# Performance work log

Hardware: AMD Instinct MI355X
Metric: run time of the kernel (lower is better)

## Reference

```python
import jax, jax.numpy as jnp
import numpy as np

N = 50000      # nodes
E = 1600000    # edges (avg degree 32)
IN = 128       # input feature dim
H = 4          # heads
C = 16         # out channels per head
NEG_SLOPE = 0.2


def setup_inputs() -> dict:
    key = jax.random.key(0)
    k = jax.random.split(key, 6)
    x = jax.random.normal(k[0], (N, IN), jnp.float32)
    edge_index = jax.random.randint(k[1], (2, E), 0, N, dtype=jnp.int32).astype(jnp.int64)
    W = jax.random.normal(k[2], (H * C, IN), jnp.float32) * (1.0 / np.sqrt(IN))
    att_src = jax.random.normal(k[3], (H, C), jnp.float32) * 0.1
    att_dst = jax.random.normal(k[4], (H, C), jnp.float32) * 0.1
    bias = jax.random.normal(k[5], (H * C,), jnp.float32) * 0.01
    return {"x": x, "edge_index": edge_index, "W": W,
            "att_src": att_src, "att_dst": att_dst, "bias": bias}


def reference(x, edge_index, W, att_src, att_dst, bias):
    # shared linear projection (PyG GATConv lin, no bias): [N, H, C]
    xp = (x @ W.T).reshape(-1, H, C)
    # per-node attention logits: [N, H]
    a_src = jnp.einsum('nhc,hc->nh', xp, att_src)
    a_dst = jnp.einsum('nhc,hc->nh', xp, att_dst)
    src, dst = edge_index[0], edge_index[1]  # messages flow src(j) -> dst(i)
    # per-edge scores: [E, H]
    e = jax.nn.leaky_relu(a_src[src] + a_dst[dst], negative_slope=NEG_SLOPE)
    # segment softmax over destination neighborhoods
    m = jax.ops.segment_max(e, dst, num_segments=N)           # [N, H]
    m = jnp.where(jnp.isfinite(m), m, 0.0)                     # empty segments
    ex = jnp.exp(e - m[dst])
    s = jax.ops.segment_sum(ex, dst, num_segments=N)           # [N, H]
    alpha = ex / (s[dst] + 1e-16)                              # [E, H]
    # weighted messages, scatter-add to destinations
    msg = (alpha[:, :, None] * xp[src]).reshape(E, H * C)      # [E, H*C]
    out = jax.ops.segment_sum(msg, dst, num_segments=N)        # [N, H*C]
    return out + bias
```

## Files before the change

kernel.cpp:

```cpp
#include <hip/hip_runtime.h>
#include <hip/hip_bf16.h>
#include <math.h>

#define N_NODES 50000
#define N_EDGES 1600000
#define IN_DIM  128
#define HC      64
#define NH      4
#define SLOTS   72
#define BSHIFT  6
#define BNODES  64
#define NB      782
#define BCAP    2432
#define EPB     2736
#define GEMM_BLOCKS 391
#define FAT_GRID 587
#define FAT_LDS 33792

__global__ __launch_bounds__(512) void gemm_bucket_kernel(
    const float* __restrict__ x, const float* __restrict__ W,
    const float* __restrict__ att_src, const float* __restrict__ att_dst,
    const int* __restrict__ ei,
    __hip_bfloat16* __restrict__ xp, float* __restrict__ a_src,
    float* __restrict__ a_dst,
    int* __restrict__ gcursor, unsigned int* __restrict__ barr) {
    extern __shared__ char smraw[];
    int tid = (int)threadIdx.x;
    int bx  = (int)blockIdx.x;

    {
        int* lcount = (int*)smraw;
        int* lbase  = lcount + NB;
        for (int j = tid; j < NB; j += 512) lcount[j] = 0;
        __syncthreads();
        int s[6], d[6], bk[6], lpos[6]; bool val[6];
#pragma unroll
        for (int u = 0; u < 6; ++u) {
            int off = u * 512 + tid;
            int e   = bx * EPB + off;
            val[u]  = (off < EPB) && (e < N_EDGES);
            int ee  = val[u] ? e : 0;
            s[u] = ei[ee];
            d[u] = ei[N_EDGES + ee];
            bk[u] = d[u] >> BSHIFT;
            if (val[u]) lpos[u] = atomicAdd(&lcount[bk[u]], 1);
        }
        __syncthreads();
        for (int j = tid; j < NB; j += 512) {
            int c = lcount[j];
            lbase[j] = (c > 0) ? atomicAdd(&gcursor[j], c) : 0;
        }
        __syncthreads();
#pragma unroll
        for (int u = 0; u < 6; ++u) {
            if (val[u]) {
                int pos = lbase[bk[u]] + lpos[u];
                if (pos < BCAP)
                    barr[(size_t)bk[u] * BCAP + pos] =
                        (unsigned)s[u] | ((unsigned)(d[u] & (BNODES - 1)) << 20);
            }
        }
    }

    if (bx < GEMM_BLOCKS) {
        __syncthreads();
        int gb = bx;
        float* Wl = (float*)smraw;
        const float4* W4 = (const float4*)W;
#pragma unroll
        for (int j = 0; j < 4; ++j) {
            int f = j * 512 + tid;
            int c = f >> 5, k4 = f & 31;
            *(float4*)&Wl[c * 132 + k4 * 4] = W4[f];
        }
        __syncthreads();

        int l = tid & 63, w = tid >> 6, q = l >> 4, i = l & 15;
        int n0 = gb * 128 + w * 16 + q * 4;
        int nj[4];
#pragma unroll
        for (int j = 0; j < 4; ++j) {
            int n = n0 + j;
            nj[j] = (n < N_NODES) ? n : N_NODES - 1;
        }
        const float* wlp = Wl + i * 132;
        float4 acc[4] = {{0,0,0,0},{0,0,0,0},{0,0,0,0},{0,0,0,0}};
        float4 xr[4], xn[4];
#pragma unroll
        for (int j = 0; j < 4; ++j) xr[j] = *(const float4*)(x + (size_t)nj[j] * IN_DIM);
#pragma unroll 2
        for (int k0 = 0; k0 < IN_DIM; k0 += 4) {
            if (k0 + 4 < IN_DIM) {
#pragma unroll
                for (int j = 0; j < 4; ++j)
                    xn[j] = *(const float4*)(x + (size_t)nj[j] * IN_DIM + k0 + 4);
            }
            float4 wl0 = *(const float4*)(wlp + 0 * 16 * 132 + k0);
            float4 wl1 = *(const float4*)(wlp + 1 * 16 * 132 + k0);
            float4 wl2 = *(const float4*)(wlp + 2 * 16 * 132 + k0);
            float4 wl3 = *(const float4*)(wlp + 3 * 16 * 132 + k0);
#pragma unroll
            for (int j = 0; j < 4; ++j) {
                float4 xv = xr[j];
                acc[j].x = fmaf(xv.x, wl0.x, fmaf(xv.y, wl0.y, fmaf(xv.z, wl0.z, fmaf(xv.w, wl0.w, acc[j].x))));
                acc[j].y = fmaf(xv.x, wl1.x, fmaf(xv.y, wl1.y, fmaf(xv.z, wl1.z, fmaf(xv.w, wl1.w, acc[j].y))));
                acc[j].z = fmaf(xv.x, wl2.x, fmaf(xv.y, wl2.y, fmaf(xv.z, wl2.z, fmaf(xv.w, wl2.w, acc[j].z))));
                acc[j].w = fmaf(xv.x, wl3.x, fmaf(xv.y, wl3.y, fmaf(xv.z, wl3.z, fmaf(xv.w, wl3.w, acc[j].w))));
            }
#pragma unroll
            for (int j = 0; j < 4; ++j) xr[j] = xn[j];
        }

        float a_s0 = att_src[i], a_s1 = att_src[16 + i], a_s2 = att_src[32 + i], a_s3 = att_src[48 + i];
        float a_d0 = att_dst[i], a_d1 = att_dst[16 + i], a_d2 = att_dst[32 + i], a_d3 = att_dst[48 + i];
#pragma unroll
        for (int j = 0; j < 4; ++j) {
            int n = n0 + j;
            if (n < N_NODES) {
                __hip_bfloat16* xw = xp + (size_t)n * HC;
                xw[i]      = __float2bfloat16(acc[j].x);
                xw[16 + i] = __float2bfloat16(acc[j].y);
                xw[32 + i] = __float2bfloat16(acc[j].z);
                xw[48 + i] = __float2bfloat16(acc[j].w);
                float4 ps, pd;
                ps.x = acc[j].x * a_s0; ps.y = acc[j].y * a_s1;
                ps.z = acc[j].z * a_s2; ps.w = acc[j].w * a_s3;
                pd.x = acc[j].x * a_d0; pd.y = acc[j].y * a_d1;
                pd.z = acc[j].z * a_d2; pd.w = acc[j].w * a_d3;
#pragma unroll
                for (int off = 1; off < 16; off <<= 1) {
                    ps.x += __shfl_xor(ps.x, off, 64); ps.y += __shfl_xor(ps.y, off, 64);
                    ps.z += __shfl_xor(ps.z, off, 64); ps.w += __shfl_xor(ps.w, off, 64);
                    pd.x += __shfl_xor(pd.x, off, 64); pd.y += __shfl_xor(pd.y, off, 64);
                    pd.z += __shfl_xor(pd.z, off, 64); pd.w += __shfl_xor(pd.w, off, 64);
                }
                if (i == 0) {
                    *(float4*)(a_src + n * NH) = ps;
                    *(float4*)(a_dst + n * NH) = pd;
                }
            }
        }
    }
}

__global__ __launch_bounds__(512) void fused_gather_kernel(
    const unsigned int* __restrict__ barr, const int* __restrict__ gcursor,
    const float* __restrict__ a_src, const float* __restrict__ a_dst,
    const __hip_bfloat16* __restrict__ xp, const float* __restrict__ bias,
    float* __restrict__ out) {
    __shared__ int lcsr[BNODES * SLOTS];
    __shared__ int deg[BNODES];
    int b = blockIdx.x, tid = (int)threadIdx.x;
    if (tid < BNODES) deg[tid] = 0;
    __syncthreads();
    int n = gcursor[b];
    n = (n < BCAP) ? n : BCAP;
    const unsigned int* src = barr + (size_t)b * BCAP;

    for (int i0 = 0; i0 < n; i0 += 2048) {
        int ibase = i0 + tid * 4;
        unsigned v[4]; bool val[4]; int dp[4], pos[4];
        if (ibase < n) {
            uint4 r = *(const uint4*)(src + ibase);
            v[0] = r.x; v[1] = r.y; v[2] = r.z; v[3] = r.w;
        } else { v[0] = v[1] = v[2] = v[3] = 0u; }
#pragma unroll
        for (int u = 0; u < 4; ++u) {
            val[u] = (ibase + u) < n;
            dp[u] = (int)(v[u] >> 20);
            if (val[u]) pos[u] = atomicAdd(&deg[dp[u]], 1);
        }
#pragma unroll
        for (int u = 0; u < 4; ++u)
            if (val[u] && pos[u] < SLOTS)
                lcsr[dp[u] * SLOTS + pos[u]] = (int)(v[u] & 0xFFFFF);
    }
    __syncthreads();

    int l = tid & 63;
    int w = tid >> 6;
    int g = l >> 3;
    int i = l & 7;
    int h = i >> 1;
    int dl = w * 8 + g;
    int dst = (b << BSHIFT) + dl;
    int dg = deg[dl];
    dg = (dg < SLOTS) ? dg : SLOTS;
    int dstc = (dst < N_NODES) ? dst : 0;
    float adh = a_dst[dstc * NH + h];

    int sreg[9];
#pragma unroll
    for (int k = 0; k < 9; ++k) sreg[k] = lcsr[dl * SLOTS + k * 8 + i];

    const unsigned short* xpi = (const unsigned short*)xp + 8 * i;
    const float* asrch = a_src + h;
    int gsel = l & 56;
    float a0=0,a1=0,a2=0,a3=0,a4=0,a5=0,a6=0,a7=0;
    float dsum = 0.f;

#pragma unroll
    for (int k = 0; k < 9; ++k) {
        if (dg > k * 8) {
            int cnt = dg - k * 8;
            int reg = sreg[k];
            int s8[8]; float g8[8]; uint4 t8[8];
#pragma unroll
            for (int u = 0; u < 8; ++u) {
                int raw = __shfl(reg, gsel | u, 64);
                s8[u] = (u < cnt) ? raw : 0;
            }
#pragma unroll
            for (int u = 0; u < 8; ++u) g8[u] = asrch[s8[u] * NH];
#pragma unroll
            for (int u = 0; u < 8; ++u)
                t8[u] = *(const uint4*)(xpi + (size_t)s8[u] * HC);
#pragma unroll
            for (int u = 0; u < 8; ++u) {
                float e = g8[u] + adh;
                e = fmaxf(e, 0.2f * e);
                float wv = (u < cnt) ? __expf(e) : 0.f;
                dsum += wv;
                uint4 t = t8[u];
                a0 = fmaf(wv, __uint_as_float(t.x << 16),          a0);
                a1 = fmaf(wv, __uint_as_float(t.x & 0xffff0000u),  a1);
                a2 = fmaf(wv, __uint_as_float(t.y << 16),          a2);
                a3 = fmaf(wv, __uint_as_float(t.y & 0xffff0000u),  a3);
                a4 = fmaf(wv, __uint_as_float(t.z << 16),          a4);
                a5 = fmaf(wv, __uint_as_float(t.z & 0xffff0000u),  a5);
                a6 = fmaf(wv, __uint_as_float(t.w << 16),          a6);
                a7 = fmaf(wv, __uint_as_float(t.w & 0xffff0000u),  a7);
            }
        }
    }
    if (dst < N_NODES) {
        float inv = 1.f / (dsum + 1e-16f);
        float4 b0 = *(const float4*)(bias + 8 * i);
        float4 b1 = *(const float4*)(bias + 8 * i + 4);
        float4 o0, o1;
        o0.x = a0 * inv + b0.x; o0.y = a1 * inv + b0.y;
        o0.z = a2 * inv + b0.z; o0.w = a3 * inv + b0.w;
        o1.x = a4 * inv + b1.x; o1.y = a5 * inv + b1.y;
        o1.z = a6 * inv + b1.z; o1.w = a7 * inv + b1.w;
        float* op = out + (size_t)dst * HC + 8 * i;
        *(float4*)op = o0;
        *(float4*)(op + 4) = o1;
    }
}

extern "C" void kernel_launch(void* const* d_in, const int* in_sizes, int n_in,
                              void* d_out, int out_size, void* d_ws, size_t ws_size,
                              hipStream_t stream) {
    const float* x       = (const float*)d_in[0];
    const int*   ei      = (const int*)d_in[1];
    const float* W       = (const float*)d_in[2];
    const float* att_src = (const float*)d_in[3];
    const float* att_dst = (const float*)d_in[4];
    const float* bias    = (const float*)d_in[5];
    float* out = (float*)d_out;

    char* ws = (char*)d_ws;
    __hip_bfloat16* xp      = (__hip_bfloat16*)(ws);
    float*          a_srcv  = (float*)(ws + 6400000);
    float*          a_dstv  = (float*)(ws + 7200000);
    int*            gcursor = (int*)  (ws + 8000000);
    unsigned int*   barr    = (unsigned int*)(ws + 8016384);

    hipMemsetAsync(gcursor, 0, NB * sizeof(int), stream);
    gemm_bucket_kernel<<<FAT_GRID, 512, FAT_LDS, stream>>>(
        x, W, att_src, att_dst, ei, xp, a_srcv, a_dstv, gcursor, barr);
    fused_gather_kernel<<<NB, 512, 0, stream>>>(barr, gcursor,
                                                a_srcv, a_dstv, xp, bias, out);
}
```

Measured before the change: 159.9 us.

## Replace two-level bucket binning with per-node global atomic slot binning

Edges are binned directly into fixed 72-slot per-destination arrays using global atomics on a per-node degree counter, in a new standalone kernel. This replaces the earlier scheme of bucket-level LDS counting, global cursor reservation and a second LDS re-binning pass inside the gather kernel. The gather kernel now just copies a ready-made slot table into LDS and reads degrees from global memory. The GEMM is split out of the fused binning kernel, so the two no longer run concurrently in one launch. The change trades many LDS atomics for 1.6M scattered global atomics and scattered 4-byte stores, and it adds an extra launch.

```diff
diff --git a/kernel.cpp b/kernel.cpp
--- a/kernel.cpp
+++ b/kernel.cpp
@@ -11,169 +11,124 @@
 #define BSHIFT  6
 #define BNODES  64
 #define NB      782
-#define BCAP    2432
-#define EPB     2736
+#define NPAD    50048
 #define GEMM_BLOCKS 391
-#define FAT_GRID 587
-#define FAT_LDS 33792
-
-__global__ __launch_bounds__(512) void gemm_bucket_kernel(
+#define GEMM_LDS 33792
+
+__global__ __launch_bounds__(256) void bin_kernel(
+    const int* __restrict__ ei, int* __restrict__ gdeg,
+    int* __restrict__ barr) {
+    int gid = (int)blockIdx.x * 256 + (int)threadIdx.x;
+    if (gid >= N_EDGES / 4) return;
+    int4 sv = ((const int4*)ei)[gid];
+    int4 dv = ((const int4*)(ei + N_EDGES))[gid];
+    int s[4] = {sv.x, sv.y, sv.z, sv.w};
+    int d[4] = {dv.x, dv.y, dv.z, dv.w};
+#pragma unroll
+    for (int u = 0; u < 4; ++u) {
+        int slot = atomicAdd(&gdeg[d[u]], 1);
+        if (slot < SLOTS)
+            barr[d[u] * SLOTS + slot] = s[u];
+    }
+}
+
+__global__ __launch_bounds__(512) void gemm_kernel(
     const float* __restrict__ x, const float* __restrict__ W,
     const float* __restrict__ att_src, const float* __restrict__ att_dst,
-    const int* __restrict__ ei,
     __hip_bfloat16* __restrict__ xp, float* __restrict__ a_src,
-    float* __restrict__ a_dst,
-    int* __restrict__ gcursor, unsigned int* __restrict__ barr) {
+    float* __restrict__ a_dst) {
     extern __shared__ char smraw[];
     int tid = (int)threadIdx.x;
-    int bx  = (int)blockIdx.x;
-
-    {
-        int* lcount = (int*)smraw;
-        int* lbase  = lcount + NB;
-        for (int j = tid; j < NB; j += 512) lcount[j] = 0;
-        __syncthreads();
-        int s[6], d[6], bk[6], lpos[6]; bool val[6];
-#pragma unroll
-        for (int u = 0; u < 6; ++u) {
-            int off = u * 512 + tid;
-            int e   = bx * EPB + off;
-            val[u]  = (off < EPB) && (e < N_EDGES);
-            int ee  = val[u] ? e : 0;
-            s[u] = ei[ee];
-            d[u] = ei[N_EDGES + ee];
-            bk[u] = d[u] >> BSHIFT;
-            if (val[u]) lpos[u] = atomicAdd(&lcount[bk[u]], 1);
-        }
-        __syncthreads();
-        for (int j = tid; j < NB; j += 512) {
-            int c = lcount[j];
-            lbase[j] = (c > 0) ? atomicAdd(&gcursor[j], c) : 0;
-        }
-        __syncthreads();
-#pragma unroll
-        for (int u = 0; u < 6; ++u) {
-            if (val[u]) {
-                int pos = lbase[bk[u]] + lpos[u];
-                if (pos < BCAP)
-                    barr[(size_t)bk[u] * BCAP + pos] =
-                        (unsigned)s[u] | ((unsigned)(d[u] & (BNODES - 1)) << 20);
-            }
-        }
-    }
-
-    if (bx < GEMM_BLOCKS) {
-        __syncthreads();
-        int gb = bx;
-        float* Wl = (float*)smraw;
-        const float4* W4 = (const float4*)W;
+    int gb  = (int)blockIdx.x;
+    float* Wl = (float*)smraw;
+    const float4* W4 = (const float4*)W;
+#pragma unroll
+    for (int j = 0; j < 4; ++j) {
+        int f = j * 512 + tid;
+        int c = f >> 5, k4 = f & 31;
+        *(float4*)&Wl[c * 132 + k4 * 4] = W4[f];
+    }
+    __syncthreads();
+
+    int l = tid & 63, w = tid >> 6, q = l >> 4, i = l & 15;
+    int n0 = gb * 128 + w * 16 + q * 4;
+    int nj[4];
+#pragma unroll
+    for (int j = 0; j < 4; ++j) {
+        int n = n0 + j;
+        nj[j] = (n < N_NODES) ? n : N_NODES - 1;
+    }
+    const float* wlp = Wl + i * 132;
+    float4 acc[4] = {{0,0,0,0},{0,0,0,0},{0,0,0,0},{0,0,0,0}};
+    float4 xr[4], xn[4];
+#pragma unroll
+    for (int j = 0; j < 4; ++j) xr[j] = *(const float4*)(x + (size_t)nj[j] * IN_DIM);
+#pragma unroll 2
+    for (int k0 = 0; k0 < IN_DIM; k0 += 4) {
+        if (k0 + 4 < IN_DIM) {
+#pragma unroll
+            for (int j = 0; j < 4; ++j)
+                xn[j] = *(const float4*)(x + (size_t)nj[j] * IN_DIM + k0 + 4);
+        }
+        float4 wl0 = *(const float4*)(wlp + 0 * 16 * 132 + k0);
+        float4 wl1 = *(const float4*)(wlp + 1 * 16 * 132 + k0);
+        float4 wl2 = *(const float4*)(wlp + 2 * 16 * 132 + k0);
+        float4 wl3 = *(const float4*)(wlp + 3 * 16 * 132 + k0);
 #pragma unroll
         for (int j = 0; j < 4; ++j) {
-            int f = j * 512 + tid;
-            int c = f >> 5, k4 = f & 31;
-            *(float4*)&Wl[c * 132 + k4 * 4] = W4[f];
-        }
-        __syncthreads();
-
-        int l = tid & 63, w = tid >> 6, q = l >> 4, i = l & 15;
-        int n0 = gb * 128 + w * 16 + q * 4;
-        int nj[4];
-#pragma unroll
-        for (int j = 0; j < 4; ++j) {
-            int n = n0 + j;
-            nj[j] = (n < N_NODES) ? n : N_NODES - 1;
-        }
-        const float* wlp = Wl + i * 132;
-        float4 acc[4] = {{0,0,0,0},{0,0,0,0},{0,0,0,0},{0,0,0,0}};
-        float4 xr[4], xn[4];
-#pragma unroll
-        for (int j = 0; j < 4; ++j) xr[j] = *(const float4*)(x + (size_t)nj[j] * IN_DIM);
-#pragma unroll 2
-        for (int k0 = 0; k0 < IN_DIM; k0 += 4) {
-            if (k0 + 4 < IN_DIM) {
-#pragma unroll
-                for (int j = 0; j < 4; ++j)
-                    xn[j] = *(const float4*)(x + (size_t)nj[j] * IN_DIM + k0 + 4);
-            }
-            float4 wl0 = *(const float4*)(wlp + 0 * 16 * 132 + k0);
-            float4 wl1 = *(const float4*)(wlp + 1 * 16 * 132 + k0);
-            float4 wl2 = *(const float4*)(wlp + 2 * 16 * 132 + k0);
-            float4 wl3 = *(const float4*)(wlp + 3 * 16 * 132 + k0);
-#pragma unroll
-            for (int j = 0; j < 4; ++j) {
-                float4 xv = xr[j];
-                acc[j].x = fmaf(xv.x, wl0.x, fmaf(xv.y, wl0.y, fmaf(xv.z, wl0.z, fmaf(xv.w, wl0.w, acc[j].x))));
-                acc[j].y = fmaf(xv.x, wl1.x, fmaf(xv.y, wl1.y, fmaf(xv.z, wl1.z, fmaf(xv.w, wl1.w, acc[j].y))));
-                acc[j].z = fmaf(xv.x, wl2.x, fmaf(xv.y, wl2.y, fmaf(xv.z, wl2.z, fmaf(xv.w, wl2.w, acc[j].z))));
-                acc[j].w = fmaf(xv.x, wl3.x, fmaf(xv.y, wl3.y, fmaf(xv.z, wl3.z, fmaf(xv.w, wl3.w, acc[j].w))));
-            }
-#pragma unroll
-            for (int j = 0; j < 4; ++j) xr[j] = xn[j];
-        }
-
-        float a_s0 = att_src[i], a_s1 = att_src[16 + i], a_s2 = att_src[32 + i], a_s3 = att_src[48 + i];
-        float a_d0 = att_dst[i], a_d1 = att_dst[16 + i], a_d2 = att_dst[32 + i], a_d3 = att_dst[48 + i];
-#pragma unroll
-        for (int j = 0; j < 4; ++j) {
-            int n = n0 + j;
-            if (n < N_NODES) {
-                __hip_bfloat16* xw = xp + (size_t)n * HC;
-                xw[i]      = __float2bfloat16(acc[j].x);
-                xw[16 + i] = __float2bfloat16(acc[j].y);
-                xw[32 + i] = __float2bfloat16(acc[j].z);
-                xw[48 + i] = __float2bfloat16(acc[j].w);
-                float4 ps, pd;
-                ps.x = acc[j].x * a_s0; ps.y = acc[j].y * a_s1;
-                ps.z = acc[j].z * a_s2; ps.w = acc[j].w * a_s3;
-                pd.x = acc[j].x * a_d0; pd.y = acc[j].y * a_d1;
-                pd.z = acc[j].z * a_d2; pd.w = acc[j].w * a_d3;
-#pragma unroll
-                for (int off = 1; off < 16; off <<= 1) {
-                    ps.x += __shfl_xor(ps.x, off, 64); ps.y += __shfl_xor(ps.y, off, 64);
-                    ps.z += __shfl_xor(ps.z, off, 64); ps.w += __shfl_xor(ps.w, off, 64);
-                    pd.x += __shfl_xor(pd.x, off, 64); pd.y += __shfl_xor(pd.y, off, 64);
-                    pd.z += __shfl_xor(pd.z, off, 64); pd.w += __shfl_xor(pd.w, off, 64);
-                }
-                if (i == 0) {
-                    *(float4*)(a_src + n * NH) = ps;
-                    *(float4*)(a_dst + n * NH) = pd;
-                }
+            float4 xv = xr[j];
+            acc[j].x = fmaf(xv.x, wl0.x, fmaf(xv.y, wl0.y, fmaf(xv.z, wl0.z, fmaf(xv.w, wl0.w, acc[j].x))));
+            acc[j].y = fmaf(xv.x, wl1.x, fmaf(xv.y, wl1.y, fmaf(xv.z, wl1.z, fmaf(xv.w, wl1.w, acc[j].y))));
+            acc[j].z = fmaf(xv.x, wl2.x, fmaf(xv.y, wl2.y, fmaf(xv.z, wl2.z, fmaf(xv.w, wl2.w, acc[j].z))));
+            acc[j].w = fmaf(xv.x, wl3.x, fmaf(xv.y, wl3.y, fmaf(xv.z, wl3.z, fmaf(xv.w, wl3.w, acc[j].w))));
+        }
+#pragma unroll
+        for (int j = 0; j < 4; ++j) xr[j] = xn[j];
+    }
+
+    float a_s0 = att_src[i], a_s1 = att_src[16 + i], a_s2 = att_src[32 + i], a_s3 = att_src[48 + i];
+    float a_d0 = att_dst[i], a_d1 = att_dst[16 + i], a_d2 = att_dst[32 + i], a_d3 = att_dst[48 + i];
+#pragma unroll
+    for (int j = 0; j < 4; ++j) {
+        int n = n0 + j;
+        if (n < N_NODES) {
+            __hip_bfloat16* xw = xp + (size_t)n * HC;
+            xw[i]      = __float2bfloat16(acc[j].x);
+            xw[16 + i] = __float2bfloat16(acc[j].y);
+            xw[32 + i] = __float2bfloat16(acc[j].z);
+            xw[48 + i] = __float2bfloat16(acc[j].w);
+            float4 ps, pd;
+            ps.x = acc[j].x * a_s0; ps.y = acc[j].y * a_s1;
+            ps.z = acc[j].z * a_s2; ps.w = acc[j].w * a_s3;
+            pd.x = acc[j].x * a_d0; pd.y = acc[j].y * a_d1;
+            pd.z = acc[j].z * a_d2; pd.w = acc[j].w * a_d3;
+#pragma unroll
+            for (int off = 1; off < 16; off <<= 1) {
+                ps.x += __shfl_xor(ps.x, off, 64); ps.y += __shfl_xor(ps.y, off, 64);
+                ps.z += __shfl_xor(ps.z, off, 64); ps.w += __shfl_xor(ps.w, off, 64);
+                pd.x += __shfl_xor(pd.x, off, 64); pd.y += __shfl_xor(pd.y, off, 64);
+                pd.z += __shfl_xor(pd.z, off, 64); pd.w += __shfl_xor(pd.w, off, 64);
+            }
+            if (i == 0) {
+                *(float4*)(a_src + n * NH) = ps;
+                *(float4*)(a_dst + n * NH) = pd;
             }
         }
     }
 }
 
 __global__ __launch_bounds__(512) void fused_gather_kernel(
-    const unsigned int* __restrict__ barr, const int* __restrict__ gcursor,
+    const int* __restrict__ barr, const int* __restrict__ gdeg,
     const float* __restrict__ a_src, const float* __restrict__ a_dst,
     const __hip_bfloat16* __restrict__ xp, const float* __restrict__ bias,
     float* __restrict__ out) {
     __shared__ int lcsr[BNODES * SLOTS];
-    __shared__ int deg[BNODES];
     int b = blockIdx.x, tid = (int)threadIdx.x;
-    if (tid < BNODES) deg[tid] = 0;
-    __syncthreads();
-    int n = gcursor[b];
-    n = (n < BCAP) ? n : BCAP;
-    const unsigned int* src = barr + (size_t)b * BCAP;
-
-    for (int i0 = 0; i0 < n; i0 += 2048) {
-        int ibase = i0 + tid * 4;
-        unsigned v[4]; bool val[4]; int dp[4], pos[4];
-        if (ibase < n) {
-            uint4 r = *(const uint4*)(src + ibase);
-            v[0] = r.x; v[1] = r.y; v[2] = r.z; v[3] = r.w;
-        } else { v[0] = v[1] = v[2] = v[3] = 0u; }
-#pragma unroll
-        for (int u = 0; u < 4; ++u) {
-            val[u] = (ibase + u) < n;
-            dp[u] = (int)(v[u] >> 20);
-            if (val[u]) pos[u] = atomicAdd(&deg[dp[u]], 1);
-        }
-#pragma unroll
-        for (int u = 0; u < 4; ++u)
-            if (val[u] && pos[u] < SLOTS)
-                lcsr[dp[u] * SLOTS + pos[u]] = (int)(v[u] & 0xFFFFF);
+    const uint4* gsrc = (const uint4*)(barr + (size_t)b * BNODES * SLOTS);
+#pragma unroll
+    for (int j = 0; j < 3; ++j) {
+        int f = j * 512 + tid;
+        if (f < (BNODES * SLOTS) / 4) ((uint4*)lcsr)[f] = gsrc[f];
     }
     __syncthreads();
 
@@ -184,7 +139,7 @@
     int h = i >> 1;
     int dl = w * 8 + g;
     int dst = (b << BSHIFT) + dl;
-    int dg = deg[dl];
+    int dg = gdeg[dst];
     dg = (dg < SLOTS) ? dg : SLOTS;
     int dstc = (dst < N_NODES) ? dst : 0;
     float adh = a_dst[dstc * NH + h];
@@ -260,15 +215,16 @@
     float* out = (float*)d_out;
 
     char* ws = (char*)d_ws;
-    __hip_bfloat16* xp      = (__hip_bfloat16*)(ws);
-    float*          a_srcv  = (float*)(ws + 6400000);
-    float*          a_dstv  = (float*)(ws + 7200000);
-    int*            gcursor = (int*)  (ws + 8000000);
-    unsigned int*   barr    = (unsigned int*)(ws + 8016384);
-
-    hipMemsetAsync(gcursor, 0, NB * sizeof(int), stream);
-    gemm_bucket_kernel<<<FAT_GRID, 512, FAT_LDS, stream>>>(
-        x, W, att_src, att_dst, ei, xp, a_srcv, a_dstv, gcursor, barr);
-    fused_gather_kernel<<<NB, 512, 0, stream>>>(barr, gcursor,
+    __hip_bfloat16* xp     = (__hip_bfloat16*)(ws);
+    float*          a_srcv = (float*)(ws + 6400000);
+    float*          a_dstv = (float*)(ws + 7200000);
+    int*            gdeg   = (int*)  (ws + 8000000);
+    int*            barr   = (int*)  (ws + 8200192);
+
+    hipMemsetAsync(gdeg, 0, NPAD * sizeof(int), stream);
+    bin_kernel<<<(N_EDGES / 4 + 255) / 256, 256, 0, stream>>>(ei, gdeg, barr);
+    gemm_kernel<<<GEMM_BLOCKS, 512, GEMM_LDS, stream>>>(
+        x, W, att_src, att_dst, xp, a_srcv, a_dstv);
+    fused_gather_kernel<<<NB, 512, 0, stream>>>(barr, gdeg,
                                                 a_srcv, a_dstv, xp, bias, out);
 }
```

After: 266.5 us. +66.7%, slower.

## Split edge binning into separate 64-block kernel with larger per-block chunks

Applied to the files above, without the earlier changes.

Moves edge bucketing out of the fused GEMM kernel into its own kernel that uses 64 blocks, each handling 25000 edges with int4 loads. Each block does a counting pass and then a scatter pass, so each block reserves one global cursor range per bucket and writes longer contiguous runs per bucket. The aim is fewer global atomics and better write locality in barr. In exchange it adds a kernel launch, serialises binning before the GEMM instead of overlapping them, reads the destination indices twice, and may underfill the GPU with only 64 blocks.

```diff
diff --git a/kernel.cpp b/kernel.cpp
--- a/kernel.cpp
+++ b/kernel.cpp
@@ -12,132 +12,140 @@
 #define BNODES  64
 #define NB      782
 #define BCAP    2432
-#define EPB     2736
+#define BIN_BLOCKS 64
+#define BIN_G   6250
+#define BIN_IT  13
 #define GEMM_BLOCKS 391
-#define FAT_GRID 587
-#define FAT_LDS 33792
-
-__global__ __launch_bounds__(512) void gemm_bucket_kernel(
+#define GEMM_LDS 33792
+
+__global__ __launch_bounds__(512) void bin_kernel(
+    const int* __restrict__ ei, int* __restrict__ gcursor,
+    unsigned int* __restrict__ barr) {
+    __shared__ int lcount[NB], lbase[NB], lcnt2[NB];
+    int tid = (int)threadIdx.x;
+    int bx  = (int)blockIdx.x;
+    for (int j = tid; j < NB; j += 512) { lcount[j] = 0; lcnt2[j] = 0; }
+    __syncthreads();
+    const int4* sp = (const int4*)ei;
+    const int4* dp = (const int4*)(ei + N_EDGES);
+    int g0 = bx * BIN_G;
+
+    for (int it = 0; it < BIN_IT; ++it) {
+        int gi = it * 512 + tid;
+        if (gi < BIN_G) {
+            int4 dv = dp[g0 + gi];
+            atomicAdd(&lcount[dv.x >> BSHIFT], 1);
+            atomicAdd(&lcount[dv.y >> BSHIFT], 1);
+            atomicAdd(&lcount[dv.z >> BSHIFT], 1);
+            atomicAdd(&lcount[dv.w >> BSHIFT], 1);
+        }
+    }
+    __syncthreads();
+    for (int j = tid; j < NB; j += 512) {
+        int c = lcount[j];
+        lbase[j] = (c > 0) ? atomicAdd(&gcursor[j], c) : 0;
+    }
+    __syncthreads();
+    for (int it = 0; it < BIN_IT; ++it) {
+        int gi = it * 512 + tid;
+        if (gi < BIN_G) {
+            int4 sv = sp[g0 + gi];
+            int4 dv = dp[g0 + gi];
+            int s[4] = {sv.x, sv.y, sv.z, sv.w};
+            int d[4] = {dv.x, dv.y, dv.z, dv.w};
+#pragma unroll
+            for (int u = 0; u < 4; ++u) {
+                int bk = d[u] >> BSHIFT;
+                int lp = atomicAdd(&lcnt2[bk], 1);
+                int pos = lbase[bk] + lp;
+                if (pos < BCAP)
+                    barr[(size_t)bk * BCAP + pos] =
+                        (unsigned)s[u] | ((unsigned)(d[u] & (BNODES - 1)) << 20);
+            }
+        }
+    }
+}
+
+__global__ __launch_bounds__(512) void gemm_kernel(
     const float* __restrict__ x, const float* __restrict__ W,
     const float* __restrict__ att_src, const float* __restrict__ att_dst,
-    const int* __restrict__ ei,
     __hip_bfloat16* __restrict__ xp, float* __restrict__ a_src,
-    float* __restrict__ a_dst,
-    int* __restrict__ gcursor, unsigned int* __restrict__ barr) {
+    float* __restrict__ a_dst) {
     extern __shared__ char smraw[];
     int tid = (int)threadIdx.x;
-    int bx  = (int)blockIdx.x;
-
-    {
-        int* lcount = (int*)smraw;
-        int* lbase  = lcount + NB;
-        for (int j = tid; j < NB; j += 512) lcount[j] = 0;
-        __syncthreads();
-        int s[6], d[6], bk[6], lpos[6]; bool val[6];
-#pragma unroll
-        for (int u = 0; u < 6; ++u) {
-            int off = u * 512 + tid;
-            int e   = bx * EPB + off;
-            val[u]  = (off < EPB) && (e < N_EDGES);
-            int ee  = val[u] ? e : 0;
-            s[u] = ei[ee];
-            d[u] = ei[N_EDGES + ee];
-            bk[u] = d[u] >> BSHIFT;
-            if (val[u]) lpos[u] = atomicAdd(&lcount[bk[u]], 1);
-        }
-        __syncthreads();
-        for (int j = tid; j < NB; j += 512) {
-            int c = lcount[j];
-            lbase[j] = (c > 0) ? atomicAdd(&gcursor[j], c) : 0;
-        }
-        __syncthreads();
-#pragma unroll
-        for (int u = 0; u < 6; ++u) {
-            if (val[u]) {
-                int pos = lbase[bk[u]] + lpos[u];
-                if (pos < BCAP)
-                    barr[(size_t)bk[u] * BCAP + pos] =
-                        (unsigned)s[u] | ((unsigned)(d[u] & (BNODES - 1)) << 20);
-            }
-        }
-    }
-
-    if (bx < GEMM_BLOCKS) {
-        __syncthreads();
-        int gb = bx;
-        float* Wl = (float*)smraw;
-        const float4* W4 = (const float4*)W;
+    int gb  = (int)blockIdx.x;
+    float* Wl = (float*)smraw;
+    const float4* W4 = (const float4*)W;
+#pragma unroll
+    for (int j = 0; j < 4; ++j) {
+        int f = j * 512 + tid;
+        int c = f >> 5, k4 = f & 31;
+        *(float4*)&Wl[c * 132 + k4 * 4] = W4[f];
+    }
+    __syncthreads();
+
+    int l = tid & 63, w = tid >> 6, q = l >> 4, i = l & 15;
+    int n0 = gb * 128 + w * 16 + q * 4;
+    int nj[4];
+#pragma unroll
+    for (int j = 0; j < 4; ++j) {
+        int n = n0 + j;
+        nj[j] = (n < N_NODES) ? n : N_NODES - 1;
+    }
+    const float* wlp = Wl + i * 132;
+    float4 acc[4] = {{0,0,0,0},{0,0,0,0},{0,0,0,0},{0,0,0,0}};
+    float4 xr[4], xn[4];
+#pragma unroll
+    for (int j = 0; j < 4; ++j) xr[j] = *(const float4*)(x + (size_t)nj[j] * IN_DIM);
+#pragma unroll 2
+    for (int k0 = 0; k0 < IN_DIM; k0 += 4) {
+        if (k0 + 4 < IN_DIM) {
+#pragma unroll
+            for (int j = 0; j < 4; ++j)
+                xn[j] = *(const float4*)(x + (size_t)nj[j] * IN_DIM + k0 + 4);
+        }
+        float4 wl0 = *(const float4*)(wlp + 0 * 16 * 132 + k0);
+        float4 wl1 = *(const float4*)(wlp + 1 * 16 * 132 + k0);
+        float4 wl2 = *(const float4*)(wlp + 2 * 16 * 132 + k0);
+        float4 wl3 = *(const float4*)(wlp + 3 * 16 * 132 + k0);
 #pragma unroll
         for (int j = 0; j < 4; ++j) {
-            int f = j * 512 + tid;
-            int c = f >> 5, k4 = f & 31;
-            *(float4*)&Wl[c * 132 + k4 * 4] = W4[f];
-        }
-        __syncthreads();
-
-        int l = tid & 63, w = tid >> 6, q = l >> 4, i = l & 15;
-        int n0 = gb * 128 + w * 16 + q * 4;
-        int nj[4];
-#pragma unroll
-        for (int j = 0; j < 4; ++j) {
-            int n = n0 + j;
-            nj[j] = (n < N_NODES) ? n : N_NODES - 1;
-        }
-        const float* wlp = Wl + i * 132;
-        float4 acc[4] = {{0,0,0,0},{0,0,0,0},{0,0,0,0},{0,0,0,0}};
-        float4 xr[4], xn[4];
-#pragma unroll
-        for (int j = 0; j < 4; ++j) xr[j] = *(const float4*)(x + (size_t)nj[j] * IN_DIM);
-#pragma unroll 2
-        for (int k0 = 0; k0 < IN_DIM; k0 += 4) {
-            if (k0 + 4 < IN_DIM) {
-#pragma unroll
-                for (int j = 0; j < 4; ++j)
-                    xn[j] = *(const float4*)(x + (size_t)nj[j] * IN_DIM + k0 + 4);
-            }
-            float4 wl0 = *(const float4*)(wlp + 0 * 16 * 132 + k0);
-            float4 wl1 = *(const float4*)(wlp + 1 * 16 * 132 + k0);
-            float4 wl2 = *(const float4*)(wlp + 2 * 16 * 132 + k0);
-            float4 wl3 = *(const float4*)(wlp + 3 * 16 * 132 + k0);
-#pragma unroll
-            for (int j = 0; j < 4; ++j) {
-                float4 xv = xr[j];
-                acc[j].x = fmaf(xv.x, wl0.x, fmaf(xv.y, wl0.y, fmaf(xv.z, wl0.z, fmaf(xv.w, wl0.w, acc[j].x))));
-                acc[j].y = fmaf(xv.x, wl1.x, fmaf(xv.y, wl1.y, fmaf(xv.z, wl1.z, fmaf(xv.w, wl1.w, acc[j].y))));
-                acc[j].z = fmaf(xv.x, wl2.x, fmaf(xv.y, wl2.y, fmaf(xv.z, wl2.z, fmaf(xv.w, wl2.w, acc[j].z))));
-                acc[j].w = fmaf(xv.x, wl3.x, fmaf(xv.y, wl3.y, fmaf(xv.z, wl3.z, fmaf(xv.w, wl3.w, acc[j].w))));
-            }
-#pragma unroll
-            for (int j = 0; j < 4; ++j) xr[j] = xn[j];
-        }
-
-        float a_s0 = att_src[i], a_s1 = att_src[16 + i], a_s2 = att_src[32 + i], a_s3 = att_src[48 + i];
-        float a_d0 = att_dst[i], a_d1 = att_dst[16 + i], a_d2 = att_dst[32 + i], a_d3 = att_dst[48 + i];
-#pragma unroll
-        for (int j = 0; j < 4; ++j) {
-            int n = n0 + j;
-            if (n < N_NODES) {
-                __hip_bfloat16* xw = xp + (size_t)n * HC;
-                xw[i]      = __float2bfloat16(acc[j].x);
-                xw[16 + i] = __float2bfloat16(acc[j].y);
-                xw[32 + i] = __float2bfloat16(acc[j].z);
-                xw[48 + i] = __float2bfloat16(acc[j].w);
-                float4 ps, pd;
-                ps.x = acc[j].x * a_s0; ps.y = acc[j].y * a_s1;
-                ps.z = acc[j].z * a_s2; ps.w = acc[j].w * a_s3;
-                pd.x = acc[j].x * a_d0; pd.y = acc[j].y * a_d1;
-                pd.z = acc[j].z * a_d2; pd.w = acc[j].w * a_d3;
-#pragma unroll
-                for (int off = 1; off < 16; off <<= 1) {
-                    ps.x += __shfl_xor(ps.x, off, 64); ps.y += __shfl_xor(ps.y, off, 64);
-                    ps.z += __shfl_xor(ps.z, off, 64); ps.w += __shfl_xor(ps.w, off, 64);
-                    pd.x += __shfl_xor(pd.x, off, 64); pd.y += __shfl_xor(pd.y, off, 64);
-                    pd.z += __shfl_xor(pd.z, off, 64); pd.w += __shfl_xor(pd.w, off, 64);
-                }
-                if (i == 0) {
-                    *(float4*)(a_src + n * NH) = ps;
-                    *(float4*)(a_dst + n * NH) = pd;
-                }
+            float4 xv = xr[j];
+            acc[j].x = fmaf(xv.x, wl0.x, fmaf(xv.y, wl0.y, fmaf(xv.z, wl0.z, fmaf(xv.w, wl0.w, acc[j].x))));
+            acc[j].y = fmaf(xv.x, wl1.x, fmaf(xv.y, wl1.y, fmaf(xv.z, wl1.z, fmaf(xv.w, wl1.w, acc[j].y))));
+            acc[j].z = fmaf(xv.x, wl2.x, fmaf(xv.y, wl2.y, fmaf(xv.z, wl2.z, fmaf(xv.w, wl2.w, acc[j].z))));
+            acc[j].w = fmaf(xv.x, wl3.x, fmaf(xv.y, wl3.y, fmaf(xv.z, wl3.z, fmaf(xv.w, wl3.w, acc[j].w))));
+        }
+#pragma unroll
+        for (int j = 0; j < 4; ++j) xr[j] = xn[j];
+    }
+
+    float a_s0 = att_src[i], a_s1 = att_src[16 + i], a_s2 = att_src[32 + i], a_s3 = att_src[48 + i];
+    float a_d0 = att_dst[i], a_d1 = att_dst[16 + i], a_d2 = att_dst[32 + i], a_d3 = att_dst[48 + i];
+#pragma unroll
+    for (int j = 0; j < 4; ++j) {
+        int n = n0 + j;
+        if (n < N_NODES) {
+            __hip_bfloat16* xw = xp + (size_t)n * HC;
+            xw[i]      = __float2bfloat16(acc[j].x);
+            xw[16 + i] = __float2bfloat16(acc[j].y);
+            xw[32 + i] = __float2bfloat16(acc[j].z);
+            xw[48 + i] = __float2bfloat16(acc[j].w);
+            float4 ps, pd;
+            ps.x = acc[j].x * a_s0; ps.y = acc[j].y * a_s1;
+            ps.z = acc[j].z * a_s2; ps.w = acc[j].w * a_s3;
+            pd.x = acc[j].x * a_d0; pd.y = acc[j].y * a_d1;
+            pd.z = acc[j].z * a_d2; pd.w = acc[j].w * a_d3;
+#pragma unroll
+            for (int off = 1; off < 16; off <<= 1) {
+                ps.x += __shfl_xor(ps.x, off, 64); ps.y += __shfl_xor(ps.y, off, 64);
+                ps.z += __shfl_xor(ps.z, off, 64); ps.w += __shfl_xor(ps.w, off, 64);
+                pd.x += __shfl_xor(pd.x, off, 64); pd.y += __shfl_xor(pd.y, off, 64);
+                pd.z += __shfl_xor(pd.z, off, 64); pd.w += __shfl_xor(pd.w, off, 64);
+            }
+            if (i == 0) {
+                *(float4*)(a_src + n * NH) = ps;
+                *(float4*)(a_dst + n * NH) = pd;
             }
         }
     }
@@ -267,8 +275,9 @@
     unsigned int*   barr    = (unsigned int*)(ws + 8016384);
 
     hipMemsetAsync(gcursor, 0, NB * sizeof(int), stream);
-    gemm_bucket_kernel<<<FAT_GRID, 512, FAT_LDS, stream>>>(
-        x, W, att_src, att_dst, ei, xp, a_srcv, a_dstv, gcursor, barr);
+    bin_kernel<<<BIN_BLOCKS, 512, 0, stream>>>(ei, gcursor, barr);
+    gemm_kernel<<<GEMM_BLOCKS, 512, GEMM_LDS, stream>>>(
+        x, W, att_src, att_dst, xp, a_srcv, a_dstv);
     fused_gather_kernel<<<NB, 512, 0, stream>>>(barr, gcursor,
                                                 a_srcv, a_dstv, xp, bias, out);
 }
```

Measured after the change: 167.8 us. 5.0% more time.
